# Optimization experiments

Measured on AMD Instinct MI355X. Metric: run time of the kernel, lower is better.

Reference implementation:

```python
import jax, jax.numpy as jnp
import numpy as np
import math

D_MODEL = 2048
N_HEADS = 16
N_KV = 4
HEAD_DIM = D_MODEL // N_HEADS          # 128
SUB = HEAD_DIM // 2                    # 64
WINDOW = 512
THETA = 10000.0
B, S = 1, 2048


def rotate_half(x):
    x1, x2 = x[..., : x.shape[-1] // 2], x[..., x.shape[-1] // 2 :]
    return jnp.concatenate([-x2, x1], axis=-1)


def setup_inputs() -> dict:
    key = jax.random.key(0)
    ks = jax.random.split(key, 6)
    std = 0.02
    x = jax.random.normal(ks[0], (B, S, D_MODEL), dtype=jnp.float32)
    Wq = jax.random.normal(ks[1], (D_MODEL, N_HEADS * HEAD_DIM), dtype=jnp.float32) * std
    Wk = jax.random.normal(ks[2], (D_MODEL, N_KV * HEAD_DIM), dtype=jnp.float32) * std
    Wv = jax.random.normal(ks[3], (D_MODEL, N_KV * HEAD_DIM), dtype=jnp.float32) * std
    Wo = jax.random.normal(ks[4], (N_HEADS * HEAD_DIM, D_MODEL), dtype=jnp.float32) * std
    lam = jnp.full((N_HEADS,), 0.1, dtype=jnp.float32)  # diff_lambda_init
    return {"x": x, "Wq": Wq, "Wk": Wk, "Wv": Wv, "Wo": Wo, "lam": lam}


def reference(x, Wq, Wk, Wv, Wo, lam):
    b, s, _ = x.shape
    # projections -> [B, H, S, hd]
    q = (x @ Wq).reshape(b, s, N_HEADS, HEAD_DIM).transpose(0, 2, 1, 3)
    k = (x @ Wk).reshape(b, s, N_KV, HEAD_DIM).transpose(0, 2, 1, 3)
    v = (x @ Wv).reshape(b, s, N_KV, HEAD_DIM).transpose(0, 2, 1, 3)

    # RoPE (position_offset = 0)
    inv_freq = 1.0 / (THETA ** (jnp.arange(0, HEAD_DIM, 2, dtype=jnp.float32) / HEAD_DIM))
    t = jnp.arange(s, dtype=jnp.float32)
    freqs = t[:, None] * inv_freq[None, :]
    emb = jnp.concatenate([freqs, freqs], axis=-1)          # [S, hd]
    cos, sin = jnp.cos(emb), jnp.sin(emb)
    q = q * cos + rotate_half(q) * sin
    k = k * cos + rotate_half(k) * sin

    # GQA: repeat-interleave kv heads (head = kv*n_rep + r)
    n_rep = N_HEADS // N_KV
    k = jnp.repeat(k, n_rep, axis=1)
    v = jnp.repeat(v, n_rep, axis=1)

    scale = 1.0 / math.sqrt(SUB)
    q1, q2 = q[..., :SUB], q[..., SUB:]
    k1, k2 = k[..., :SUB], k[..., SUB:]
    a1 = jnp.einsum("bhqd,bhkd->bhqk", q1, k1) * scale
    a2 = jnp.einsum("bhqd,bhkd->bhqk", q2, k2) * scale

    # causal + sliding-window mask
    row = jnp.arange(s)[:, None]
    col = jnp.arange(s)[None, :]
    allowed = (col <= row) & (col >= row - WINDOW + 1)
    neg = jnp.where(allowed, 0.0, -jnp.inf).astype(a1.dtype)
    a1 = a1 + neg
    a2 = a2 + neg

    p1 = jax.nn.softmax(a1.astype(jnp.float32), axis=-1).astype(x.dtype)
    p2 = jax.nn.softmax(a2.astype(jnp.float32), axis=-1).astype(x.dtype)

    diff = jax.nn.relu(p1 - lam[None, :, None, None] * p2)
    diff = diff / (diff.sum(axis=-1, keepdims=True) + 1e-6)

    out = jnp.einsum("bhqk,bhkd->bhqd", diff, v)            # [B,H,S,hd]
    out = out.transpose(0, 2, 1, 3).reshape(b, s, N_HEADS * HEAD_DIM)
    return out @ Wo
```

## Files before the change

### kernel.cpp

```cpp
#include <hip/hip_runtime.h>

typedef unsigned short u16;
typedef __attribute__((ext_vector_type(8))) short s8b;
typedef __attribute__((ext_vector_type(4))) float f4;

static __device__ __forceinline__ float b2f(u16 u){
  return __uint_as_float(((unsigned int)u) << 16);
}
static __device__ __forceinline__ u16 f2b(float f){
  unsigned int u = __float_as_uint(f);
  u = (u + 0x7FFFu + ((u >> 16) & 1u)) >> 16;
  return (u16)u;
}
static __device__ __forceinline__ f4 mfma16(s8b a, s8b b, f4 c){
  return __builtin_amdgcn_mfma_f32_16x16x32_bf16(a, b, c, 0, 0, 0);
}
static __device__ __forceinline__ s8b load8(const float* p){
  float4 a = ((const float4*)p)[0];
  float4 b = ((const float4*)p)[1];
  s8b r;
  r[0] = (short)f2b(a.x); r[1] = (short)f2b(a.y);
  r[2] = (short)f2b(a.z); r[3] = (short)f2b(a.w);
  r[4] = (short)f2b(b.x); r[5] = (short)f2b(b.y);
  r[6] = (short)f2b(b.z); r[7] = (short)f2b(b.w);
  return r;
}
static __device__ __forceinline__ void gload16(const u16* g, u16* l){
  __builtin_amdgcn_global_load_lds((const __attribute__((address_space(1))) void*)g,
                                   (__attribute__((address_space(3))) void*)l,
                                   16, 0, 0);
}

__global__ void convert_k(const float* __restrict__ in, u16* __restrict__ out,
                          int n8){
  const int i = blockIdx.x * blockDim.x + threadIdx.x;
  if (i < n8) ((s8b*)out)[i] = load8(in + (size_t)i * 8);
}

__global__ void transpose_k(const float* __restrict__ in, u16* __restrict__ out,
                            int K, int N){
  __shared__ u16 tile[32][33];
  const int n0 = blockIdx.x << 5, k0 = blockIdx.y << 5;
  const int tx = threadIdx.x, ty = threadIdx.y;
  #pragma unroll
  for (int i = ty; i < 32; i += 8)
    tile[i][tx] = f2b(in[(size_t)(k0 + i) * N + n0 + tx]);
  __syncthreads();
  #pragma unroll
  for (int i = ty; i < 32; i += 8)
    out[(size_t)(n0 + i) * K + k0 + tx] = tile[tx][i];
}

__global__ void transpose3_k(const float* __restrict__ Wq,
                             const float* __restrict__ Wk,
                             const float* __restrict__ Wv,
                             u16* __restrict__ out){
  __shared__ u16 tile[32][33];
  int bx = blockIdx.x;
  const float* src; int N; int rowoff;
  if (bx < 64)      { src = Wq; N = 2048; rowoff = 0; }
  else if (bx < 80) { src = Wk; N = 512;  rowoff = 2048; bx -= 64; }
  else              { src = Wv; N = 512;  rowoff = 2560; bx -= 80; }
  const int n0 = bx << 5, k0 = blockIdx.y << 5;
  const int tx = threadIdx.x, ty = threadIdx.y;
  #pragma unroll
  for (int i = ty; i < 32; i += 8)
    tile[i][tx] = f2b(src[(size_t)(k0 + i) * N + n0 + tx]);
  __syncthreads();
  #pragma unroll
  for (int i = ty; i < 32; i += 8)
    out[(size_t)(rowoff + n0 + i) * 2048 + k0 + tx] = tile[tx][i];
}

template <int MODE>
__global__ __launch_bounds__(512) void gemm8(const u16* __restrict__ A,
                                             const u16* __restrict__ Bt,
                                             u16* __restrict__ Cq,
                                             u16* __restrict__ Ck,
                                             u16* __restrict__ Cv,
                                             float* __restrict__ Cf,
                                             int M, int K){
  __shared__ __align__(16) u16 As[2][128 * 32];
  __shared__ __align__(16) u16 Bs[2][128 * 32];
  const int n0 = blockIdx.x << 7;
  const int m0 = blockIdx.y << 7;
  const int tid = threadIdx.x;
  const int wave = tid >> 6, lane = tid & 63;
  const int quad = lane >> 4, ln = lane & 15;
  const int wr = (wave >> 2) << 6;
  const int wc = (wave & 3) << 5;
  const int lr = tid >> 2, lc = (tid & 3) << 3;

  f4 acc[4][2];
  #pragma unroll
  for (int i = 0; i < 4; ++i)
    #pragma unroll
    for (int j = 0; j < 2; ++j){ f4 z = {0.f,0.f,0.f,0.f}; acc[i][j] = z; }

  const u16* ag = A  + (size_t)(m0 + lr) * K + lc;
  const u16* bg = Bt + (size_t)(n0 + lr) * K + lc;
  const int NT = K >> 5;

  gload16(ag, As[0] + tid * 8);
  gload16(bg, Bs[0] + tid * 8);

  for (int t = 0; t < NT; ++t){
    const int cur = t & 1;
    const int kn = ((t + 1) < NT ? (t + 1) : t) << 5;
    gload16(ag + kn, As[cur ^ 1] + tid * 8);
    gload16(bg + kn, Bs[cur ^ 1] + tid * 8);
    asm volatile("s_waitcnt vmcnt(2)" ::: "memory");
    __builtin_amdgcn_s_barrier();
    s8b af[4], bf[2];
    #pragma unroll
    for (int i = 0; i < 4; ++i) af[i] = *(const s8b*)&As[cur][(wr + i*16 + ln)*32 + quad*8];
    #pragma unroll
    for (int j = 0; j < 2; ++j) bf[j] = *(const s8b*)&Bs[cur][(wc + j*16 + ln)*32 + quad*8];
    #pragma unroll
    for (int i = 0; i < 4; ++i)
      #pragma unroll
      for (int j = 0; j < 2; ++j)
        acc[i][j] = mfma16(af[i], bf[j], acc[i][j]);
    asm volatile("s_waitcnt lgkmcnt(0)" ::: "memory");
    __builtin_amdgcn_s_barrier();
  }
  #pragma unroll
  for (int i = 0; i < 4; ++i)
    #pragma unroll
    for (int j = 0; j < 2; ++j)
      #pragma unroll
      for (int r = 0; r < 4; ++r){
        const int row = m0 + wr + i*16 + quad*4 + r;
        const int col = n0 + wc + j*16 + ln;
        const float v = acc[i][j][r];
        if (MODE == 1){
          Cf[(size_t)row * 2048 + col] = v;
        } else {
          if (col < 2048)       Cq[(size_t)row * 2048 + col]          = f2b(v);
          else if (col < 2560)  Ck[(size_t)row * 512  + (col - 2048)] = f2b(v);
          else                  Cv[(size_t)(col - 2560) * 2048 + row] = f2b(v);
        }
      }
}

__global__ void rope2_k(u16* __restrict__ q, u16* __restrict__ k){
  const int s = blockIdx.x;
  #pragma unroll
  for (int it = 0; it < 5; ++it){
    const int p = it * 256 + threadIdx.x;
    int hh, i; u16* base;
    if (p < 1024){
      hh = p >> 6; i = p & 63;
      base = q + (size_t)s * 2048 + hh * 128 + i;
    } else {
      const int pp = p - 1024;
      hh = pp >> 6; i = pp & 63;
      base = k + (size_t)s * 512 + hh * 128 + i;
    }
    const float inv = __expf(-(float)i * 0.14391157f);
    const float ang = (float)s * inv;
    float c, sn;
    sincosf(ang, &sn, &c);
    const float x1 = b2f(base[0]), x2 = b2f(base[64]);
    base[0]  = f2b(x1 * c - x2 * sn);
    base[64] = f2b(x2 * c + x1 * sn);
  }
}

__global__ __launch_bounds__(256) void attn_k(const u16* __restrict__ q,
                                              const u16* __restrict__ kk,
                                              const u16* __restrict__ vt,
                                              const float* __restrict__ lam,
                                              u16* __restrict__ ctx){
  const int h   = blockIdx.x >> 5;
  const int qt  = blockIdx.x & 31;
  const int qt0 = qt << 6;
  const int tid = threadIdx.x;
  const int w = tid >> 6, lane = tid & 63;
  const int quad = lane >> 4, ln = lane & 15;
  const int kvh = h >> 2;
  const float lam_h = lam[h];
  const float scale = 0.125f;
  const int qbw = qt0 + (w << 4);

  __shared__ __align__(16) u16 Ks[2][32 * 128];
  __shared__ __align__(16) u16 Vs[2][128 * 32];
  __shared__ __align__(16) u16 p_lds[4][2][16][40];

  s8b qf[4];
  {
    const u16* qrow = q + (size_t)(qbw + ln) * 2048 + h * 128 + quad * 8;
    #pragma unroll
    for (int s = 0; s < 4; ++s) qf[s] = *(const s8b*)(qrow + s * 32);
  }

  const int tlo = (qt0 > 511) ? ((qt0 - 511) >> 5) : 0;
  const int thi = ((qt0 + 63) >> 5) + 1;

#define STAGE_K(buf, t) {                                                         \
    const int kc = (t) << 5;                                                      \
    _Pragma("unroll")                                                             \
    for (int i_ = 0; i_ < 2; ++i_){                                               \
      const int slot = tid + i_ * 256;                                            \
      const int row_ = slot >> 4, c16_ = slot & 15;                               \
      const u16* src_ = kk + (size_t)(kc + row_) * 512 + kvh * 128                \
                        + ((c16_ ^ (row_ & 7)) << 3);                             \
      gload16(src_, &Ks[buf][slot * 8]);                                          \
    } }
#define STAGE_V(buf, t) {                                                         \
    const int kc = (t) << 5;                                                      \
    _Pragma("unroll")                                                             \
    for (int i_ = 0; i_ < 2; ++i_){                                               \
      const int slot = tid + i_ * 256;                                            \
      const int row_ = slot >> 2, c16_ = slot & 3;                                \
      const u16* src_ = vt + (size_t)(kvh * 128 + row_) * 2048 + kc               \
                        + ((c16_ ^ (row_ & 3)) << 3);                             \
      gload16(src_, &Vs[buf][slot * 8]);                                          \
    } }

  float l1[4] = {0.f,0.f,0.f,0.f}, l2[4] = {0.f,0.f,0.f,0.f};
  STAGE_K(0, tlo);
  asm volatile("s_waitcnt vmcnt(0)" ::: "memory");
  __builtin_amdgcn_s_barrier();
  for (int t = tlo; t < thi; ++t){
    const int cur = (t - tlo) & 1;
    if (t + 1 < thi){
      STAGE_K(cur ^ 1, t + 1);
      asm volatile("s_waitcnt vmcnt(2)" ::: "memory");
    } else {
      asm volatile("s_waitcnt vmcnt(0)" ::: "memory");
    }
    __builtin_amdgcn_s_barrier();
    const int kcol0 = t << 5;
    if (kcol0 <= qbw + 15 && kcol0 + 31 >= qbw - 511){
      #pragma unroll
      for (int sub = 0; sub < 2; ++sub){
        const int krow = (sub*16 + ln) * 128;
        s8b kf0 = *(const s8b*)&Ks[cur][krow + (((quad +  0) ^ (ln & 7)) << 3)];
        s8b kf1 = *(const s8b*)&Ks[cur][krow + (((quad +  4) ^ (ln & 7)) << 3)];
        s8b kf2 = *(const s8b*)&Ks[cur][krow + (((quad +  8) ^ (ln & 7)) << 3)];
        s8b kf3 = *(const s8b*)&Ks[cur][krow + (((quad + 12) ^ (ln & 7)) << 3)];
        f4 z = {0.f,0.f,0.f,0.f};
        f4 s1 = mfma16(qf[1], kf1, mfma16(qf[0], kf0, z));
        f4 s2 = mfma16(qf[3], kf3, mfma16(qf[2], kf2, z));
        const int col = kcol0 + sub*16 + ln;
        #pragma unroll
        for (int r = 0; r < 4; ++r){
          const int row = qbw + quad*4 + r;
          if (col <= row && col > row - 512){
            l1[r] += __expf(s1[r] * scale);
            l2[r] += __expf(s2[r] * scale);
          }
        }
      }
    }
    asm volatile("s_waitcnt lgkmcnt(0)" ::: "memory");
    __builtin_amdgcn_s_barrier();
  }
  #pragma unroll
  for (int r = 0; r < 4; ++r){
    #pragma unroll
    for (int off = 1; off < 16; off <<= 1){
      l1[r] += __shfl_xor(l1[r], off, 16);
      l2[r] += __shfl_xor(l2[r], off, 16);
    }
  }
  float il1[4], il2[4];
  #pragma unroll
  for (int r = 0; r < 4; ++r){ il1[r] = 1.f / l1[r]; il2[r] = 1.f / l2[r]; }

  f4 acc[8];
  #pragma unroll
  for (int dt = 0; dt < 8; ++dt){ f4 z = {0.f,0.f,0.f,0.f}; acc[dt] = z; }
  float den[4] = {0.f,0.f,0.f,0.f};

  STAGE_K(0, tlo);
  STAGE_V(0, tlo);
  asm volatile("s_waitcnt vmcnt(0)" ::: "memory");
  __builtin_amdgcn_s_barrier();
  for (int t = tlo; t < thi; ++t){
    const int cur = (t - tlo) & 1;
    if (t + 1 < thi){
      STAGE_K(cur ^ 1, t + 1);
      STAGE_V(cur ^ 1, t + 1);
      asm volatile("s_waitcnt vmcnt(4)" ::: "memory");
    } else {
      asm volatile("s_waitcnt vmcnt(0)" ::: "memory");
    }
    __builtin_amdgcn_s_barrier();
    const int kcol0 = t << 5;
    if (kcol0 <= qbw + 15 && kcol0 + 31 >= qbw - 511){
      #pragma unroll
      for (int sub = 0; sub < 2; ++sub){
        const int krow = (sub*16 + ln) * 128;
        s8b kf0 = *(const s8b*)&Ks[cur][krow + (((quad +  0) ^ (ln & 7)) << 3)];
        s8b kf1 = *(const s8b*)&Ks[cur][krow + (((quad +  4) ^ (ln & 7)) << 3)];
        s8b kf2 = *(const s8b*)&Ks[cur][krow + (((quad +  8) ^ (ln & 7)) << 3)];
        s8b kf3 = *(const s8b*)&Ks[cur][krow + (((quad + 12) ^ (ln & 7)) << 3)];
        f4 z = {0.f,0.f,0.f,0.f};
        f4 s1 = mfma16(qf[1], kf1, mfma16(qf[0], kf0, z));
        f4 s2 = mfma16(qf[3], kf3, mfma16(qf[2], kf2, z));
        const int col = kcol0 + sub*16 + ln;
        #pragma unroll
        for (int r = 0; r < 4; ++r){
          const int row = qbw + quad*4 + r;
          float pd = 0.f;
          if (col <= row && col > row - 512){
            const float p1 = __expf(s1[r] * scale) * il1[r];
            const float p2 = __expf(s2[r] * scale) * il2[r];
            pd = fmaxf(p1 - lam_h * p2, 0.f);
          }
          den[r] += pd;
          p_lds[w][(t - tlo) & 1][quad*4 + r][sub*16 + ln] = f2b(pd);
        }
      }
      s8b pf = *(const s8b*)&p_lds[w][(t - tlo) & 1][ln][quad * 8];
      #pragma unroll
      for (int dt = 0; dt < 8; ++dt){
        s8b vf = *(const s8b*)&Vs[cur][(dt*16 + ln)*32 + ((quad ^ (ln & 3)) << 3)];
        acc[dt] = mfma16(pf, vf, acc[dt]);
      }
    }
    asm volatile("s_waitcnt lgkmcnt(0)" ::: "memory");
    __builtin_amdgcn_s_barrier();
  }

  #pragma unroll
  for (int r = 0; r < 4; ++r)
    #pragma unroll
    for (int off = 1; off < 16; off <<= 1)
      den[r] += __shfl_xor(den[r], off, 16);
  #pragma unroll
  for (int r = 0; r < 4; ++r){
    const float dn = 1.f / (den[r] + 1e-6f);
    const int row = qbw + quad*4 + r;
    u16* orow = ctx + (size_t)row * 2048 + h * 128 + ln;
    #pragma unroll
    for (int dt = 0; dt < 8; ++dt)
      orow[dt * 16] = f2b(acc[dt][r] * dn);
  }
#undef STAGE_K
#undef STAGE_V
}

extern "C" void kernel_launch(void* const* d_in, const int* in_sizes, int n_in,
                              void* d_out, int out_size, void* d_ws, size_t ws_size,
                              hipStream_t stream){
  (void)in_sizes; (void)n_in; (void)out_size; (void)ws_size;
  const float* x   = (const float*)d_in[0];
  const float* Wq  = (const float*)d_in[1];
  const float* Wk  = (const float*)d_in[2];
  const float* Wv  = (const float*)d_in[3];
  const float* Wo  = (const float*)d_in[4];
  const float* lam = (const float*)d_in[5];
  char* ws = (char*)d_ws;
  u16* WT  = (u16*)(ws);
  u16* kb  = (u16*)(ws + (size_t)(13u << 20));
  u16* vtb = (u16*)(ws + (size_t)(15u << 20));
  u16* ctx = WT;
  u16* WoT = (u16*)(ws + (size_t)( 8u << 20));
  u16* xb  = (u16*)d_out;
  u16* qb  = (u16*)((char*)d_out + (size_t)(8u << 20));
  float* out = (float*)d_out;

  const dim3 tb(32, 8);
  convert_k<<<2048, 256, 0, stream>>>(x, xb, 2048 * 2048 / 8);
  transpose3_k<<<dim3(96, 64), tb, 0, stream>>>(Wq, Wk, Wv, WT);
  gemm8<0><<<dim3(24, 16), 512, 0, stream>>>(xb, WT, qb, kb, vtb, nullptr, 2048, 2048);
  rope2_k<<<2048, 256, 0, stream>>>(qb, kb);
  attn_k<<<512, 256, 0, stream>>>(qb, kb, vtb, lam, ctx);
  transpose_k<<<dim3(64, 64), tb, 0, stream>>>(Wo, WoT, 2048, 2048);
  gemm8<1><<<dim3(16, 16), 512, 0, stream>>>(ctx, WoT, nullptr, nullptr, nullptr, out, 2048, 2048);
}
```

Measured before the change: 258.2 us.

## Cache softmax exponentials in registers and swizzle GEMM/V LDS layouts

The attention kernel now keeps the exponentials from the first pass in fp16 registers, with the loop fully unrolled over 18 tiles. This lets the second pass skip re-staging K, recomputing QK^T with MFMA, and re-evaluating exp. The values are pre-scaled by 1/16 so they fit in fp16. The GEMM loader and the V staging also gain XOR swizzles on their LDS columns to reduce bank conflicts. In exchange it uses many more VGPRs (36 h8 vectors), which may lower occupancy, and fp16 caching adds rounding error.

```diff
diff --git a/kernel.cpp b/kernel.cpp
--- a/kernel.cpp
+++ b/kernel.cpp
@@ -3,6 +3,7 @@
 typedef unsigned short u16;
 typedef __attribute__((ext_vector_type(8))) short s8b;
 typedef __attribute__((ext_vector_type(4))) float f4;
+typedef __attribute__((ext_vector_type(8))) _Float16 h8;
 
 static __device__ __forceinline__ float b2f(u16 u){
   return __uint_as_float(((unsigned int)u) << 16);
@@ -89,7 +90,8 @@
   const int quad = lane >> 4, ln = lane & 15;
   const int wr = (wave >> 2) << 6;
   const int wc = (wave & 3) << 5;
-  const int lr = tid >> 2, lc = (tid & 3) << 3;
+  const int lr = tid >> 2;
+  const int lc = (((tid & 3) ^ ((tid >> 3) & 3)) << 3);
 
   f4 acc[4][2];
   #pragma unroll
@@ -100,6 +102,7 @@
   const u16* ag = A  + (size_t)(m0 + lr) * K + lc;
   const u16* bg = Bt + (size_t)(n0 + lr) * K + lc;
   const int NT = K >> 5;
+  const int rsw = ((ln >> 1) & 3) << 3;
 
   gload16(ag, As[0] + tid * 8);
   gload16(bg, Bs[0] + tid * 8);
@@ -113,9 +116,11 @@
     __builtin_amdgcn_s_barrier();
     s8b af[4], bf[2];
     #pragma unroll
-    for (int i = 0; i < 4; ++i) af[i] = *(const s8b*)&As[cur][(wr + i*16 + ln)*32 + quad*8];
-    #pragma unroll
-    for (int j = 0; j < 2; ++j) bf[j] = *(const s8b*)&Bs[cur][(wc + j*16 + ln)*32 + quad*8];
+    for (int i = 0; i < 4; ++i)
+      af[i] = *(const s8b*)&As[cur][(wr + i*16 + ln)*32 + ((quad*8) ^ rsw)];
+    #pragma unroll
+    for (int j = 0; j < 2; ++j)
+      bf[j] = *(const s8b*)&Bs[cur][(wc + j*16 + ln)*32 + ((quad*8) ^ rsw)];
     #pragma unroll
     for (int i = 0; i < 4; ++i)
       #pragma unroll
@@ -214,16 +219,21 @@
       const int slot = tid + i_ * 256;                                            \
       const int row_ = slot >> 2, c16_ = slot & 3;                                \
       const u16* src_ = vt + (size_t)(kvh * 128 + row_) * 2048 + kc               \
-                        + ((c16_ ^ (row_ & 3)) << 3);                             \
+                        + ((c16_ ^ ((row_ >> 1) & 3)) << 3);                      \
       gload16(src_, &Vs[buf][slot * 8]);                                          \
     } }
 
+  h8 eh[18], eh2[18];
   float l1[4] = {0.f,0.f,0.f,0.f}, l2[4] = {0.f,0.f,0.f,0.f};
+
   STAGE_K(0, tlo);
   asm volatile("s_waitcnt vmcnt(0)" ::: "memory");
   __builtin_amdgcn_s_barrier();
-  for (int t = tlo; t < thi; ++t){
-    const int cur = (t - tlo) & 1;
+  #pragma unroll
+  for (int tt = 0; tt < 18; ++tt){
+    const int t = tlo + tt;
+    if (t >= thi) continue;
+    const int cur = tt & 1;
     if (t + 1 < thi){
       STAGE_K(cur ^ 1, t + 1);
       asm volatile("s_waitcnt vmcnt(2)" ::: "memory");
@@ -244,14 +254,18 @@
         f4 s1 = mfma16(qf[1], kf1, mfma16(qf[0], kf0, z));
         f4 s2 = mfma16(qf[3], kf3, mfma16(qf[2], kf2, z));
         const int col = kcol0 + sub*16 + ln;
+        h8 ev;
         #pragma unroll
         for (int r = 0; r < 4; ++r){
           const int row = qbw + quad*4 + r;
-          if (col <= row && col > row - 512){
-            l1[r] += __expf(s1[r] * scale);
-            l2[r] += __expf(s2[r] * scale);
-          }
+          const bool ok = (col <= row) && (col > row - 512);
+          const float a = ok ? __expf(s1[r] * scale) * 0.0625f : 0.f;
+          const float b = ok ? __expf(s2[r] * scale) * 0.0625f : 0.f;
+          l1[r] += a; l2[r] += b;
+          ev[2*r]   = (_Float16)a;
+          ev[2*r+1] = (_Float16)b;
         }
+        if (sub == 0) eh[tt] = ev; else eh2[tt] = ev;
       }
     }
     asm volatile("s_waitcnt lgkmcnt(0)" ::: "memory");
@@ -274,16 +288,17 @@
   for (int dt = 0; dt < 8; ++dt){ f4 z = {0.f,0.f,0.f,0.f}; acc[dt] = z; }
   float den[4] = {0.f,0.f,0.f,0.f};
 
-  STAGE_K(0, tlo);
   STAGE_V(0, tlo);
   asm volatile("s_waitcnt vmcnt(0)" ::: "memory");
   __builtin_amdgcn_s_barrier();
-  for (int t = tlo; t < thi; ++t){
-    const int cur = (t - tlo) & 1;
+  #pragma unroll
+  for (int tt = 0; tt < 18; ++tt){
+    const int t = tlo + tt;
+    if (t >= thi) continue;
+    const int cur = tt & 1;
     if (t + 1 < thi){
-      STAGE_K(cur ^ 1, t + 1);
       STAGE_V(cur ^ 1, t + 1);
-      asm volatile("s_waitcnt vmcnt(4)" ::: "memory");
+      asm volatile("s_waitcnt vmcnt(2)" ::: "memory");
     } else {
       asm volatile("s_waitcnt vmcnt(0)" ::: "memory");
     }
@@ -292,32 +307,20 @@
     if (kcol0 <= qbw + 15 && kcol0 + 31 >= qbw - 511){
       #pragma unroll
       for (int sub = 0; sub < 2; ++sub){
-        const int krow = (sub*16 + ln) * 128;
-        s8b kf0 = *(const s8b*)&Ks[cur][krow + (((quad +  0) ^ (ln & 7)) << 3)];
-        s8b kf1 = *(const s8b*)&Ks[cur][krow + (((quad +  4) ^ (ln & 7)) << 3)];
-        s8b kf2 = *(const s8b*)&Ks[cur][krow + (((quad +  8) ^ (ln & 7)) << 3)];
-        s8b kf3 = *(const s8b*)&Ks[cur][krow + (((quad + 12) ^ (ln & 7)) << 3)];
-        f4 z = {0.f,0.f,0.f,0.f};
-        f4 s1 = mfma16(qf[1], kf1, mfma16(qf[0], kf0, z));
-        f4 s2 = mfma16(qf[3], kf3, mfma16(qf[2], kf2, z));
-        const int col = kcol0 + sub*16 + ln;
+        const h8 ev = (sub == 0) ? eh[tt] : eh2[tt];
         #pragma unroll
         for (int r = 0; r < 4; ++r){
-          const int row = qbw + quad*4 + r;
-          float pd = 0.f;
-          if (col <= row && col > row - 512){
-            const float p1 = __expf(s1[r] * scale) * il1[r];
-            const float p2 = __expf(s2[r] * scale) * il2[r];
-            pd = fmaxf(p1 - lam_h * p2, 0.f);
-          }
+          const float a = (float)ev[2*r];
+          const float b = (float)ev[2*r+1];
+          const float pd = fmaxf(a * il1[r] - lam_h * (b * il2[r]), 0.f);
           den[r] += pd;
-          p_lds[w][(t - tlo) & 1][quad*4 + r][sub*16 + ln] = f2b(pd);
+          p_lds[w][cur][quad*4 + r][sub*16 + ln] = f2b(pd);
         }
       }
-      s8b pf = *(const s8b*)&p_lds[w][(t - tlo) & 1][ln][quad * 8];
+      s8b pf = *(const s8b*)&p_lds[w][cur][ln][quad * 8];
       #pragma unroll
       for (int dt = 0; dt < 8; ++dt){
-        s8b vf = *(const s8b*)&Vs[cur][(dt*16 + ln)*32 + ((quad ^ (ln & 3)) << 3)];
+        s8b vf = *(const s8b*)&Vs[cur][(dt*16 + ln)*32 + (((quad) ^ ((ln >> 1) & 3)) << 3)];
         acc[dt] = mfma16(pf, vf, acc[dt]);
       }
     }
```

New measurement: 242.7 us. -6.0%, faster.
